# Kernel tuning notes

Hardware: AMD Instinct MI355X
Metric: run time of the kernel (lower is better)

## Reference

```python
import jax, jax.numpy as jnp
import numpy as np

N = 50000
E = 800000
IN = 256
HID = 64
H12 = 4
LAT = 32
NEG_SLOPE = 0.2


def gat_conv(x, src, dst, W, a_src, a_dst, b, heads, out_ch, concat):
    """PyG GATConv (eval mode, add_self_loops already applied to src/dst).
    x: [N, F_in]; src/dst: [Etot]; W: [F_in, heads*out_ch]; a_*: [heads, out_ch]; b: bias.
    Returns (out, alpha[Etot, heads])."""
    n = x.shape[0]
    h = (x @ W).reshape(n, heads, out_ch)                 # [N,H,C]
    e_src = (h * a_src).sum(-1)                           # [N,H]
    e_dst = (h * a_dst).sum(-1)                           # [N,H]
    e = jax.nn.leaky_relu(e_src[src] + e_dst[dst], NEG_SLOPE)   # [Etot,H]
    emax = jax.ops.segment_max(e, dst, num_segments=n)
    ee = jnp.exp(e - emax[dst])
    denom = jax.ops.segment_sum(ee, dst, num_segments=n)
    alpha = ee / (denom[dst] + 1e-16)                     # segment softmax over incoming edges
    msg = h[src] * alpha[:, :, None]                      # [Etot,H,C]
    out = jax.ops.segment_sum(msg, dst, num_segments=n)   # [N,H,C]
    out = out.reshape(n, heads * out_ch) if concat else out.mean(axis=1)
    return out + b, alpha


def setup_inputs() -> dict:
    key = jax.random.key(0)
    ks = jax.random.split(key, 20)
    s = 0.1
    inp = {
        "x": jax.random.normal(ks[0], (N, IN), jnp.float32),
        "edge_index": jax.random.randint(ks[1], (2, E), 0, N, jnp.int32),
        "W1": jax.random.normal(ks[2], (IN, H12 * HID), jnp.float32) * s,
        "a1s": jax.random.normal(ks[3], (H12, HID), jnp.float32) * s,
        "a1d": jax.random.normal(ks[4], (H12, HID), jnp.float32) * s,
        "b1": jnp.zeros((H12 * HID,), jnp.float32),
        "W2": jax.random.normal(ks[5], (H12 * HID, H12 * HID), jnp.float32) * s,
        "a2s": jax.random.normal(ks[6], (H12, HID), jnp.float32) * s,
        "a2d": jax.random.normal(ks[7], (H12, HID), jnp.float32) * s,
        "b2": jnp.zeros((HID,), jnp.float32),
        "Wm": jax.random.normal(ks[8], (HID, LAT), jnp.float32) * s,
        "ams": jax.random.normal(ks[9], (1, LAT), jnp.float32) * s,
        "amd": jax.random.normal(ks[10], (1, LAT), jnp.float32) * s,
        "bm": jnp.zeros((LAT,), jnp.float32),
        # log_std head
        "Ws": jax.random.normal(ks[11], (HID, LAT), jnp.float32) * s,
        "ass": jax.random.normal(ks[12], (1, LAT), jnp.float32) * s,
        "asd": jax.random.normal(ks[13], (1, LAT), jnp.float32) * s,
        "bs": jnp.zeros((LAT,), jnp.float32),
    }
    return inp


def reference(x, edge_index, W1, a1s, a1d, b1, W2, a2s, a2d, b2,
              Wm, ams, amd, bm, Ws, ass, asd, bs):
    # GATConv adds self loops by default
    loops = jnp.arange(N, dtype=edge_index.dtype)
    src = jnp.concatenate([edge_index[0], loops])
    dst = jnp.concatenate([edge_index[1], loops])

    h1, a_w1 = gat_conv(x, src, dst, W1, a1s, a1d, b1, H12, HID, True)
    h1 = jax.nn.relu(h1)
    h2, a_w2 = gat_conv(h1, src, dst, W2, a2s, a2d, b2, H12, HID, False)
    h2 = jax.nn.relu(h2)  # dropout is identity in eval mode
    z_mean, a_wm = gat_conv(h2, src, dst, Wm, ams, amd, bm, 1, LAT, False)
    z_log_std, a_ws = gat_conv(h2, src, dst, Ws, ass, asd, bs, 1, LAT, False)
    return (z_mean, z_log_std, a_w1, a_w2, a_wm, a_ws)
```

## Files before the change

### kernel.cpp

```cpp
#include <hip/hip_runtime.h>
#include <cstdint>
#include <cstddef>

#define NN 50000
#define EE 800000
#define ETOT 850000
#define NEG_SLOPE 0.2f

typedef _Float16 f16;
typedef __attribute__((ext_vector_type(4))) _Float16 f16x4;
typedef __attribute__((ext_vector_type(8))) _Float16 f16x8;
typedef __attribute__((ext_vector_type(4))) float f32x4;


__global__ __launch_bounds__(256) void deg_kernel(const int* __restrict__ ei, int* __restrict__ deg) {
    int e = blockIdx.x * 256 + threadIdx.x;
    if (e >= ETOT) return;
    int d = (e < EE) ? ei[EE + e] : (e - EE);
    atomicAdd(&deg[d], 1);
}

__global__ __launch_bounds__(256) void scan1_kernel(const int* __restrict__ deg, int* __restrict__ offs,
                                                    int* __restrict__ bsum, int n) {
    __shared__ int sh[256];
    int i = blockIdx.x * 256 + threadIdx.x;
    int v = (i < n) ? deg[i] : 0;
    sh[threadIdx.x] = v;
    __syncthreads();
    for (int off = 1; off < 256; off <<= 1) {
        int t = (threadIdx.x >= off) ? sh[threadIdx.x - off] : 0;
        __syncthreads();
        sh[threadIdx.x] += t;
        __syncthreads();
    }
    if (i < n) offs[i] = sh[threadIdx.x] - v;
    if (threadIdx.x == 255) bsum[blockIdx.x] = sh[255];
}

__global__ __launch_bounds__(256) void scan2_kernel(int* __restrict__ bsum, int nb) {
    __shared__ int sh[256];
    int v = (threadIdx.x < nb) ? bsum[threadIdx.x] : 0;
    sh[threadIdx.x] = v;
    __syncthreads();
    for (int off = 1; off < 256; off <<= 1) {
        int t = (threadIdx.x >= off) ? sh[threadIdx.x - off] : 0;
        __syncthreads();
        sh[threadIdx.x] += t;
        __syncthreads();
    }
    if (threadIdx.x < nb) bsum[threadIdx.x] = sh[threadIdx.x] - v;
}

__global__ __launch_bounds__(256) void scan3_kernel(const int* __restrict__ bsum, int* __restrict__ offs,
                                                    int* __restrict__ cursor, int n) {
    int i = blockIdx.x * 256 + threadIdx.x;
    if (i < n) {
        int o = offs[i] + bsum[blockIdx.x];
        offs[i] = o;
        cursor[i] = o;
    }
}

__global__ __launch_bounds__(256) void fill_kernel(const int* __restrict__ ei, int* __restrict__ cursor,
                                                   int* __restrict__ csrc) {
    int e = blockIdx.x * 256 + threadIdx.x;
    if (e >= ETOT) return;
    int d, s;
    if (e < EE) { s = ei[e]; d = ei[EE + e]; } else { s = e - EE; d = e - EE; }
    int p = atomicAdd(&cursor[d], 1);
    csrc[p] = s;
}


template<int K, int NH, bool AF32>
__global__ __launch_bounds__(256) void mfma_gemm_fused(
    const void* __restrict__ Ap, const f16* __restrict__ Bt, f16* __restrict__ C,
    const float* __restrict__ aS, const float* __restrict__ aD,
    float* __restrict__ es, float* __restrict__ ed, int M, int N) {
    int w = threadIdx.x >> 6, lane = threadIdx.x & 63;
    int m0 = blockIdx.y * 128 + w * 32;
    int n0 = blockIdx.x * 64;
    int r = lane & 15, kb = lane >> 4;
    int ar0 = m0 + r;       if (ar0 > M - 1) ar0 = M - 1;
    int ar1 = m0 + 16 + r;  if (ar1 > M - 1) ar1 = M - 1;
    f32x4 acc[2][4] = {};
    const float* Af = (const float*)Ap;
    const f16*   Ah = (const f16*)Ap;
    size_t a0off = (size_t)ar0 * K + kb * 8;
    size_t a1off = (size_t)ar1 * K + kb * 8;
    const f16* bbase = Bt + (size_t)(n0 + r) * K + kb * 8;
    for (int k0 = 0; k0 < K; k0 += 32) {
        f16x8 a0, a1;
        if constexpr (AF32) {
            float4 l0 = *(const float4*)(Af + a0off + k0);
            float4 h0 = *(const float4*)(Af + a0off + k0 + 4);
            float4 l1 = *(const float4*)(Af + a1off + k0);
            float4 h1 = *(const float4*)(Af + a1off + k0 + 4);
            a0[0]=(f16)l0.x; a0[1]=(f16)l0.y; a0[2]=(f16)l0.z; a0[3]=(f16)l0.w;
            a0[4]=(f16)h0.x; a0[5]=(f16)h0.y; a0[6]=(f16)h0.z; a0[7]=(f16)h0.w;
            a1[0]=(f16)l1.x; a1[1]=(f16)l1.y; a1[2]=(f16)l1.z; a1[3]=(f16)l1.w;
            a1[4]=(f16)h1.x; a1[5]=(f16)h1.y; a1[6]=(f16)h1.z; a1[7]=(f16)h1.w;
        } else {
            a0 = *(const f16x8*)(Ah + a0off + k0);
            a1 = *(const f16x8*)(Ah + a1off + k0);
        }
#pragma unroll
        for (int ni = 0; ni < 4; ++ni) {
            f16x8 b = *(const f16x8*)(bbase + (size_t)ni * 16 * K + k0);
            acc[0][ni] = __builtin_amdgcn_mfma_f32_16x16x32_f16(a0, b, acc[0][ni], 0, 0, 0);
            acc[1][ni] = __builtin_amdgcn_mfma_f32_16x16x32_f16(a1, b, acc[1][ni], 0, 0, 0);
        }
    }
    float aSl[4], aDl[4];
#pragma unroll
    for (int ni = 0; ni < 4; ++ni) {
        aSl[ni] = aS[n0 + ni * 16 + r];
        aDl[ni] = aD[n0 + ni * 16 + r];
    }
#pragma unroll
    for (int mi = 0; mi < 2; ++mi) {
#pragma unroll
        for (int i = 0; i < 4; ++i) {
            int row = m0 + mi * 16 + kb * 4 + i;
            bool ok = row < M;
            if (ok) {
#pragma unroll
                for (int ni = 0; ni < 4; ++ni)
                    C[(size_t)row * N + n0 + ni * 16 + r] = (f16)acc[mi][ni][i];
            }
            if constexpr (NH == 4) {
                float pes = acc[mi][0][i] * aSl[0] + acc[mi][1][i] * aSl[1] + acc[mi][2][i] * aSl[2] + acc[mi][3][i] * aSl[3];
                float ped = acc[mi][0][i] * aDl[0] + acc[mi][1][i] * aDl[1] + acc[mi][2][i] * aDl[2] + acc[mi][3][i] * aDl[3];
#pragma unroll
                for (int off = 1; off < 16; off <<= 1) {
                    pes += __shfl_xor(pes, off);
                    ped += __shfl_xor(ped, off);
                }
                if (r == 0 && ok) {
                    es[(size_t)row * 4 + blockIdx.x] = pes;
                    ed[(size_t)row * 4 + blockIdx.x] = ped;
                }
            } else {
                float p0s = acc[mi][0][i] * aSl[0] + acc[mi][1][i] * aSl[1];
                float p1s = acc[mi][2][i] * aSl[2] + acc[mi][3][i] * aSl[3];
                float p0d = acc[mi][0][i] * aDl[0] + acc[mi][1][i] * aDl[1];
                float p1d = acc[mi][2][i] * aDl[2] + acc[mi][3][i] * aDl[3];
#pragma unroll
                for (int off = 1; off < 16; off <<= 1) {
                    p0s += __shfl_xor(p0s, off);
                    p1s += __shfl_xor(p1s, off);
                    p0d += __shfl_xor(p0d, off);
                    p1d += __shfl_xor(p1d, off);
                }
                if (r == 0 && ok) {
                    es[(size_t)row * 2 + 0] = p0s;
                    es[(size_t)row * 2 + 1] = p1s;
                    ed[(size_t)row * 2 + 0] = p0d;
                    ed[(size_t)row * 2 + 1] = p1d;
                }
            }
        }
    }
}


__global__ __launch_bounds__(256) void packw_kernel(const float* __restrict__ W1, const float* __restrict__ W2,
                                                    const float* __restrict__ Wm, const float* __restrict__ Ws,
                                                    const float* __restrict__ ams, const float* __restrict__ ass,
                                                    const float* __restrict__ amd, const float* __restrict__ asd,
                                                    f16* __restrict__ Wt1, f16* __restrict__ Wt2,
                                                    f16* __restrict__ Wtms,
                                                    float* __restrict__ aS, float* __restrict__ aD) {
    int i = blockIdx.x * 256 + threadIdx.x;
    if (i < 65536) {
        int n = i >> 8, k = i & 255;
        Wt1[(size_t)n * 256 + k] = (f16)W1[(size_t)k * 256 + n];
        Wt2[(size_t)n * 256 + k] = (f16)W2[(size_t)k * 256 + n];
    }
    if (i < 4096) {
        int c = i >> 6, k = i & 63;
        float v = (c < 32) ? Wm[k * 32 + c] : Ws[k * 32 + (c - 32)];
        Wtms[(size_t)c * 64 + k] = (f16)v;
    }
    if (i < 64) {
        aS[i] = (i < 32) ? ams[i] : ass[i - 32];
        aD[i] = (i < 32) ? amd[i] : asd[i - 32];
    }
}

__device__ __forceinline__ float leaky(float v) { return v > 0.f ? v : NEG_SLOPE * v; }


__global__ __launch_bounds__(256) void alpha_all_kernel(
    const int* __restrict__ ei,
    const float* __restrict__ es1, const float* __restrict__ ed1, const float* __restrict__ inv1,
    const float* __restrict__ es2, const float* __restrict__ ed2, const float* __restrict__ inv2,
    const float* __restrict__ esms, const float* __restrict__ edms, const float* __restrict__ invms,
    float* __restrict__ aw1, float* __restrict__ aw2,
    float* __restrict__ awm, float* __restrict__ aws) {
    int e = blockIdx.x * 256 + threadIdx.x;
    if (e >= ETOT) return;
    int s, d;
    if (e < EE) { s = ei[e]; d = ei[EE + e]; } else { s = e - EE; d = e - EE; }
    {
        float4 esv = *(const float4*)(es1 + (size_t)s * 4);
        float4 edv = *(const float4*)(ed1 + (size_t)d * 4);
        float4 iv  = *(const float4*)(inv1 + (size_t)d * 4);
        float4 r;
        r.x = __expf(leaky(esv.x + edv.x)) * iv.x;
        r.y = __expf(leaky(esv.y + edv.y)) * iv.y;
        r.z = __expf(leaky(esv.z + edv.z)) * iv.z;
        r.w = __expf(leaky(esv.w + edv.w)) * iv.w;
        *(float4*)(aw1 + (size_t)e * 4) = r;
    }
    {
        float4 esv = *(const float4*)(es2 + (size_t)s * 4);
        float4 edv = *(const float4*)(ed2 + (size_t)d * 4);
        float4 iv  = *(const float4*)(inv2 + (size_t)d * 4);
        float4 r;
        r.x = __expf(leaky(esv.x + edv.x)) * iv.x;
        r.y = __expf(leaky(esv.y + edv.y)) * iv.y;
        r.z = __expf(leaky(esv.z + edv.z)) * iv.z;
        r.w = __expf(leaky(esv.w + edv.w)) * iv.w;
        *(float4*)(aw2 + (size_t)e * 4) = r;
    }
    {
        float2 esv = *(const float2*)(esms + (size_t)s * 2);
        float2 edv = *(const float2*)(edms + (size_t)d * 2);
        float2 iv  = *(const float2*)(invms + (size_t)d * 2);
        awm[e] = __expf(leaky(esv.x + edv.x)) * iv.x;
        aws[e] = __expf(leaky(esv.y + edv.y)) * iv.y;
    }
}


__global__ __launch_bounds__(128) void agg_concat_kernel(
    const f16* __restrict__ H, const float* __restrict__ es, const float* __restrict__ ed,
    const int* __restrict__ offs, const int* __restrict__ csrc,
    const float* __restrict__ bias, f16* __restrict__ out, float* __restrict__ invout) {
    int wave = threadIdx.x >> 6, lane = threadIdx.x & 63;
    int n = blockIdx.x * 2 + wave;
    if (n >= NN) return;
    int start = offs[n];
    int end = (n + 1 < NN) ? offs[n + 1] : ETOT;
    int deg = end - start;
    int h16 = lane >> 4, sub = lane & 15;
    float edh = ed[n * 4 + h16];
    float dsum = 0.f;
    for (int j = sub; j < deg; j += 16) {
        int s = csrc[start + j];
        dsum += __expf(leaky(es[s * 4 + h16] + edh));
    }
    for (int off = 1; off < 16; off <<= 1) dsum += __shfl_xor(dsum, off);
    float inv = 1.f / (dsum + 1e-16f);
    if (sub == 0) invout[n * 4 + h16] = inv;
    int half = lane >> 5;
    int l5 = lane & 31;
    int hh = l5 >> 3;
    int c8 = l5 * 8;
    float invh = __shfl(inv, hh << 4);
    float edhh = __shfl(edh, hh << 4);
    float accv[8] = {};
    int j = half;
    for (; j + 6 < deg; j += 8) {
        int p0 = start + j, p1 = start + j + 2, p2 = start + j + 4, p3 = start + j + 6;
        int s0 = csrc[p0], s1 = csrc[p1], s2 = csrc[p2], s3 = csrc[p3];
        float a0 = __expf(leaky(es[s0 * 4 + hh] + edhh)) * invh;
        float a1 = __expf(leaky(es[s1 * 4 + hh] + edhh)) * invh;
        float a2 = __expf(leaky(es[s2 * 4 + hh] + edhh)) * invh;
        float a3 = __expf(leaky(es[s3 * 4 + hh] + edhh)) * invh;
        f16x8 v0 = *(const f16x8*)(H + (size_t)s0 * 256 + c8);
        f16x8 v1 = *(const f16x8*)(H + (size_t)s1 * 256 + c8);
        f16x8 v2 = *(const f16x8*)(H + (size_t)s2 * 256 + c8);
        f16x8 v3 = *(const f16x8*)(H + (size_t)s3 * 256 + c8);
#pragma unroll
        for (int k = 0; k < 8; ++k)
            accv[k] += a0 * (float)v0[k] + a1 * (float)v1[k] + a2 * (float)v2[k] + a3 * (float)v3[k];
    }
    for (; j < deg; j += 2) {
        int s0 = csrc[start + j];
        float a0 = __expf(leaky(es[s0 * 4 + hh] + edhh)) * invh;
        f16x8 v0 = *(const f16x8*)(H + (size_t)s0 * 256 + c8);
#pragma unroll
        for (int k = 0; k < 8; ++k) accv[k] += a0 * (float)v0[k];
    }
#pragma unroll
    for (int k = 0; k < 8; ++k) accv[k] += __shfl_xor(accv[k], 32);
    if (lane < 32) {
        f16x8 r;
#pragma unroll
        for (int k = 0; k < 8; ++k) r[k] = (f16)fmaxf(accv[k] + bias[c8 + k], 0.f);
        *(f16x8*)(out + (size_t)n * 256 + c8) = r;
    }
}


__global__ __launch_bounds__(128) void agg_mean_kernel(
    const f16* __restrict__ H, const float* __restrict__ es, const float* __restrict__ ed,
    const int* __restrict__ offs, const int* __restrict__ csrc,
    const float* __restrict__ bias, f16* __restrict__ out, float* __restrict__ invout) {
    int wave = threadIdx.x >> 6, lane = threadIdx.x & 63;
    int n = blockIdx.x * 2 + wave;
    if (n >= NN) return;
    int start = offs[n];
    int end = (n + 1 < NN) ? offs[n + 1] : ETOT;
    int deg = end - start;
    int h16 = lane >> 4, sub = lane & 15;
    float edh = ed[n * 4 + h16];
    float dsum = 0.f;
    for (int j = sub; j < deg; j += 16) {
        int s = csrc[start + j];
        dsum += __expf(leaky(es[s * 4 + h16] + edh));
    }
    for (int off = 1; off < 16; off <<= 1) dsum += __shfl_xor(dsum, off);
    float inv = 1.f / (dsum + 1e-16f);
    if (sub == 0) invout[n * 4 + h16] = inv;
    int half = lane >> 5;
    int l5 = lane & 31;
    int hh = l5 >> 3;
    int c8 = l5 * 8;
    float invh = __shfl(inv, hh << 4);
    float edhh = __shfl(edh, hh << 4);
    float accv[8] = {};
    int j = half;
    for (; j + 6 < deg; j += 8) {
        int p0 = start + j, p1 = start + j + 2, p2 = start + j + 4, p3 = start + j + 6;
        int s0 = csrc[p0], s1 = csrc[p1], s2 = csrc[p2], s3 = csrc[p3];
        float a0 = __expf(leaky(es[s0 * 4 + hh] + edhh)) * invh;
        float a1 = __expf(leaky(es[s1 * 4 + hh] + edhh)) * invh;
        float a2 = __expf(leaky(es[s2 * 4 + hh] + edhh)) * invh;
        float a3 = __expf(leaky(es[s3 * 4 + hh] + edhh)) * invh;
        f16x8 v0 = *(const f16x8*)(H + (size_t)s0 * 256 + c8);
        f16x8 v1 = *(const f16x8*)(H + (size_t)s1 * 256 + c8);
        f16x8 v2 = *(const f16x8*)(H + (size_t)s2 * 256 + c8);
        f16x8 v3 = *(const f16x8*)(H + (size_t)s3 * 256 + c8);
#pragma unroll
        for (int k = 0; k < 8; ++k)
            accv[k] += a0 * (float)v0[k] + a1 * (float)v1[k] + a2 * (float)v2[k] + a3 * (float)v3[k];
    }
    for (; j < deg; j += 2) {
        int s0 = csrc[start + j];
        float a0 = __expf(leaky(es[s0 * 4 + hh] + edhh)) * invh;
        f16x8 v0 = *(const f16x8*)(H + (size_t)s0 * 256 + c8);
#pragma unroll
        for (int k = 0; k < 8; ++k) accv[k] += a0 * (float)v0[k];
    }
#pragma unroll
    for (int k = 0; k < 8; ++k) {
        accv[k] += __shfl_xor(accv[k], 8);
        accv[k] += __shfl_xor(accv[k], 16);
        accv[k] += __shfl_xor(accv[k], 32);
    }
    if (lane < 8) {
        f16x8 r;
#pragma unroll
        for (int k = 0; k < 8; ++k) r[k] = (f16)fmaxf(accv[k] * 0.25f + bias[lane * 8 + k], 0.f);
        *(f16x8*)(out + (size_t)n * 64 + lane * 8) = r;
    }
}


__global__ __launch_bounds__(128) void agg_ms_kernel(
    const f16* __restrict__ H, const float* __restrict__ es, const float* __restrict__ ed,
    const int* __restrict__ offs, const int* __restrict__ csrc,
    const float* __restrict__ bm, const float* __restrict__ bs,
    float* __restrict__ zmean, float* __restrict__ zlog, float* __restrict__ invout) {
    int wave = threadIdx.x >> 6, lane = threadIdx.x & 63;
    int n = blockIdx.x * 2 + wave;
    if (n >= NN) return;
    int start = offs[n];
    int end = (n + 1 < NN) ? offs[n + 1] : ETOT;
    int deg = end - start;
    int g = lane >> 5, sub = lane & 31;
    float edg = ed[n * 2 + g];
    float dsum = 0.f;
    for (int j = sub; j < deg; j += 32) {
        int s = csrc[start + j];
        dsum += __expf(leaky(es[s * 2 + g] + edg));
    }
    for (int off = 1; off < 32; off <<= 1) dsum += __shfl_xor(dsum, off);
    float inv = 1.f / (dsum + 1e-16f);
    if (sub == 0) invout[n * 2 + g] = inv;
    int slot = lane >> 3;
    int le = lane & 7;
    int g2 = le >> 2;
    int c8 = le * 8;
    float invg = __shfl(inv, g2 << 5);
    float edg2 = __shfl(edg, g2 << 5);
    float accv[8] = {};
    for (int j = slot; j < deg; j += 8) {
        int p = start + j;
        int s = csrc[p];
        float a = __expf(leaky(es[s * 2 + g2] + edg2)) * invg;
        f16x8 v = *(const f16x8*)(H + (size_t)s * 64 + c8);
#pragma unroll
        for (int k = 0; k < 8; ++k) accv[k] += a * (float)v[k];
    }
#pragma unroll
    for (int k = 0; k < 8; ++k) {
        accv[k] += __shfl_xor(accv[k], 8);
        accv[k] += __shfl_xor(accv[k], 16);
        accv[k] += __shfl_xor(accv[k], 32);
    }
    if (lane < 4) {
        float4 r0, r1;
        int cb = lane * 8;
        r0.x = accv[0] + bm[cb + 0]; r0.y = accv[1] + bm[cb + 1];
        r0.z = accv[2] + bm[cb + 2]; r0.w = accv[3] + bm[cb + 3];
        r1.x = accv[4] + bm[cb + 4]; r1.y = accv[5] + bm[cb + 5];
        r1.z = accv[6] + bm[cb + 6]; r1.w = accv[7] + bm[cb + 7];
        *(float4*)(zmean + (size_t)n * 32 + cb) = r0;
        *(float4*)(zmean + (size_t)n * 32 + cb + 4) = r1;
    } else if (lane < 8) {
        float4 r0, r1;
        int cb = (lane - 4) * 8;
        r0.x = accv[0] + bs[cb + 0]; r0.y = accv[1] + bs[cb + 1];
        r0.z = accv[2] + bs[cb + 2]; r0.w = accv[3] + bs[cb + 3];
        r1.x = accv[4] + bs[cb + 4]; r1.y = accv[5] + bs[cb + 5];
        r1.z = accv[6] + bs[cb + 6]; r1.w = accv[7] + bs[cb + 7];
        *(float4*)(zlog + (size_t)n * 32 + cb) = r0;
        *(float4*)(zlog + (size_t)n * 32 + cb + 4) = r1;
    }
}


extern "C" void kernel_launch(void* const* d_in, const int* in_sizes, int n_in,
                              void* d_out, int out_size, void* d_ws, size_t ws_size,
                              hipStream_t stream) {
    const float* x   = (const float*)d_in[0];
    const int*   ei  = (const int*)d_in[1];
    const float* W1  = (const float*)d_in[2];
    const float* a1s = (const float*)d_in[3];
    const float* a1d = (const float*)d_in[4];
    const float* b1  = (const float*)d_in[5];
    const float* W2  = (const float*)d_in[6];
    const float* a2s = (const float*)d_in[7];
    const float* a2d = (const float*)d_in[8];
    const float* b2  = (const float*)d_in[9];
    const float* Wm  = (const float*)d_in[10];
    const float* ams = (const float*)d_in[11];
    const float* amd = (const float*)d_in[12];
    const float* bm  = (const float*)d_in[13];
    const float* Ws  = (const float*)d_in[14];
    const float* ass = (const float*)d_in[15];
    const float* asd = (const float*)d_in[16];
    const float* bs  = (const float*)d_in[17];

    float* out = (float*)d_out;
    float* zmean = out;
    float* zlog  = out + 1600000;
    float* a_w1  = out + 3200000;
    float* a_w2  = out + 6600000;
    float* a_wm  = out + 10000000;
    float* a_ws_o = out + 10850000;

    float* ws = (float*)d_ws;
    size_t o = 0;
    f16*   Hh   = (f16*)(ws + o); o += (size_t)NN * 128;
    f16*   h1h  = (f16*)(ws + o); o += (size_t)NN * 128;
    f16*   h2h  = (f16*)(ws + o); o += (size_t)NN * 32;
    float* es1  = ws + o; o += NN * 4;
    float* ed1  = ws + o; o += NN * 4;
    float* es2  = ws + o; o += NN * 4;
    float* ed2  = ws + o; o += NN * 4;
    float* esms = ws + o; o += NN * 2;
    float* edms = ws + o; o += NN * 2;
    float* inv1 = ws + o; o += NN * 4;
    float* inv2 = ws + o; o += NN * 4;
    float* invms= ws + o; o += NN * 2;
    f16*   Wt1  = (f16*)(ws + o); o += 32768;
    f16*   Wt2  = (f16*)(ws + o); o += 32768;
    f16*   Wtms = (f16*)(ws + o); o += 2048;
    float* aSms = ws + o; o += 64;
    float* aDms = ws + o; o += 64;
    int* deg    = (int*)(ws + o); o += NN;
    int* offs   = (int*)(ws + o); o += NN;
    int* cursor = (int*)(ws + o); o += NN;
    int* csrc   = (int*)(ws + o); o += ETOT;

    const int edgeBlocks = (ETOT + 255) / 256;
    const int nodeBlocks = (NN + 255) / 256;
    const int aggBlocks  = (NN + 1) / 2;

    hipMemsetAsync(deg, 0, NN * sizeof(int), stream);
    deg_kernel<<<edgeBlocks, 256, 0, stream>>>(ei, deg);
    scan1_kernel<<<nodeBlocks, 256, 0, stream>>>(deg, offs, cursor , NN);
    scan2_kernel<<<1, 256, 0, stream>>>(cursor, nodeBlocks);
    scan3_kernel<<<nodeBlocks, 256, 0, stream>>>(cursor, offs, deg , NN);
    fill_kernel<<<edgeBlocks, 256, 0, stream>>>(ei, deg, csrc);

    packw_kernel<<<256, 256, 0, stream>>>(W1, W2, Wm, Ws, ams, ass, amd, asd, Wt1, Wt2, Wtms, aSms, aDms);

    dim3 gg1(4, (NN + 127) / 128);
    dim3 gg3(1, (NN + 127) / 128);
    mfma_gemm_fused<256, 4, true><<<gg1, 256, 0, stream>>>(x, Wt1, Hh, a1s, a1d, es1, ed1, NN, 256);
    agg_concat_kernel<<<aggBlocks, 128, 0, stream>>>(Hh, es1, ed1, offs, csrc, b1, h1h, inv1);

    mfma_gemm_fused<256, 4, false><<<gg1, 256, 0, stream>>>(h1h, Wt2, Hh, a2s, a2d, es2, ed2, NN, 256);
    agg_mean_kernel<<<aggBlocks, 128, 0, stream>>>(Hh, es2, ed2, offs, csrc, b2, h2h, inv2);

    mfma_gemm_fused<64, 2, false><<<gg3, 256, 0, stream>>>(h2h, Wtms, Hh, aSms, aDms, esms, edms, NN, 64);
    agg_ms_kernel<<<aggBlocks, 128, 0, stream>>>(Hh, esms, edms, offs, csrc, bm, bs,
                                                 zmean, zlog, invms);

    alpha_all_kernel<<<edgeBlocks, 256, 0, stream>>>(ei, es1, ed1, inv1, es2, ed2, inv2,
                                                     esms, edms, invms, a_w1, a_w2, a_wm, a_ws_o);
}
```

Baseline: 545.1 us.

## Fuse per-layer alpha output into next GEMM grid and interleave ed/inv storage

The monolithic alpha kernel that ran after all layers is split up. Layer-1 and layer-2 attention weights are now computed by extra blocks appended to the next layer's GEMM grid, so that edge work overlaps with the MFMA GEMM. The ed and inv arrays are interleaved per node, so one cache line serves both gathers. Aggregation kernels drop to one wave per block. The cost is a larger GEMM launch with branch-divergent block roles, and smaller blocks that raise block-scheduling overhead.

```diff
diff --git a/kernel.cpp b/kernel.cpp
--- a/kernel.cpp
+++ b/kernel.cpp
@@ -8,7 +8,6 @@
 #define NEG_SLOPE 0.2f
 
 typedef _Float16 f16;
-typedef __attribute__((ext_vector_type(4))) _Float16 f16x4;
 typedef __attribute__((ext_vector_type(8))) _Float16 f16x8;
 typedef __attribute__((ext_vector_type(4))) float f32x4;
 
@@ -71,12 +70,34 @@
     csrc[p] = s;
 }
 
-
-template<int K, int NH, bool AF32>
+__device__ __forceinline__ float leaky(float v) { return v > 0.f ? v : NEG_SLOPE * v; }
+
+
+template<int K, int NH, bool AF32, int ALPHA_NH>
 __global__ __launch_bounds__(256) void mfma_gemm_fused(
     const void* __restrict__ Ap, const f16* __restrict__ Bt, f16* __restrict__ C,
     const float* __restrict__ aS, const float* __restrict__ aD,
-    float* __restrict__ es, float* __restrict__ ed, int M, int N) {
+    float* __restrict__ es, float* __restrict__ edi, int M, int N, int RB,
+    const int* __restrict__ ei, const float* __restrict__ esA,
+    const float* __restrict__ ediA, float* __restrict__ awA) {
+    if ((int)blockIdx.y >= RB) {
+        if constexpr (ALPHA_NH == 4) {
+            int e = (((int)blockIdx.y - RB) * (int)gridDim.x + (int)blockIdx.x) * 256 + (int)threadIdx.x;
+            if (e >= ETOT) return;
+            int s, d;
+            if (e < EE) { s = ei[e]; d = ei[EE + e]; } else { s = e - EE; d = e - EE; }
+            float4 esv = *(const float4*)(esA + (size_t)s * 4);
+            float4 edv = *(const float4*)(ediA + (size_t)d * 8);
+            float4 iv  = *(const float4*)(ediA + (size_t)d * 8 + 4);
+            float4 r;
+            r.x = __expf(leaky(esv.x + edv.x)) * iv.x;
+            r.y = __expf(leaky(esv.y + edv.y)) * iv.y;
+            r.z = __expf(leaky(esv.z + edv.z)) * iv.z;
+            r.w = __expf(leaky(esv.w + edv.w)) * iv.w;
+            *(float4*)(awA + (size_t)e * 4) = r;
+        }
+        return;
+    }
     int w = threadIdx.x >> 6, lane = threadIdx.x & 63;
     int m0 = blockIdx.y * 128 + w * 32;
     int n0 = blockIdx.x * 64;
@@ -138,7 +159,7 @@
                 }
                 if (r == 0 && ok) {
                     es[(size_t)row * 4 + blockIdx.x] = pes;
-                    ed[(size_t)row * 4 + blockIdx.x] = ped;
+                    edi[(size_t)row * 8 + blockIdx.x] = ped;
                 }
             } else {
                 float p0s = acc[mi][0][i] * aSl[0] + acc[mi][1][i] * aSl[1];
@@ -155,8 +176,8 @@
                 if (r == 0 && ok) {
                     es[(size_t)row * 2 + 0] = p0s;
                     es[(size_t)row * 2 + 1] = p1s;
-                    ed[(size_t)row * 2 + 0] = p0d;
-                    ed[(size_t)row * 2 + 1] = p1d;
+                    edi[(size_t)row * 4 + 0] = p0d;
+                    edi[(size_t)row * 4 + 1] = p1d;
                 }
             }
         }
@@ -188,64 +209,33 @@
     }
 }
 
-__device__ __forceinline__ float leaky(float v) { return v > 0.f ? v : NEG_SLOPE * v; }
-
-
-__global__ __launch_bounds__(256) void alpha_all_kernel(
-    const int* __restrict__ ei,
-    const float* __restrict__ es1, const float* __restrict__ ed1, const float* __restrict__ inv1,
-    const float* __restrict__ es2, const float* __restrict__ ed2, const float* __restrict__ inv2,
-    const float* __restrict__ esms, const float* __restrict__ edms, const float* __restrict__ invms,
-    float* __restrict__ aw1, float* __restrict__ aw2,
-    float* __restrict__ awm, float* __restrict__ aws) {
+
+__global__ __launch_bounds__(256) void alpha_ms_kernel(const int* __restrict__ ei, const float* __restrict__ es,
+                                                       const float* __restrict__ edi,
+                                                       float* __restrict__ awm, float* __restrict__ aws) {
     int e = blockIdx.x * 256 + threadIdx.x;
     if (e >= ETOT) return;
     int s, d;
     if (e < EE) { s = ei[e]; d = ei[EE + e]; } else { s = e - EE; d = e - EE; }
-    {
-        float4 esv = *(const float4*)(es1 + (size_t)s * 4);
-        float4 edv = *(const float4*)(ed1 + (size_t)d * 4);
-        float4 iv  = *(const float4*)(inv1 + (size_t)d * 4);
-        float4 r;
-        r.x = __expf(leaky(esv.x + edv.x)) * iv.x;
-        r.y = __expf(leaky(esv.y + edv.y)) * iv.y;
-        r.z = __expf(leaky(esv.z + edv.z)) * iv.z;
-        r.w = __expf(leaky(esv.w + edv.w)) * iv.w;
-        *(float4*)(aw1 + (size_t)e * 4) = r;
-    }
-    {
-        float4 esv = *(const float4*)(es2 + (size_t)s * 4);
-        float4 edv = *(const float4*)(ed2 + (size_t)d * 4);
-        float4 iv  = *(const float4*)(inv2 + (size_t)d * 4);
-        float4 r;
-        r.x = __expf(leaky(esv.x + edv.x)) * iv.x;
-        r.y = __expf(leaky(esv.y + edv.y)) * iv.y;
-        r.z = __expf(leaky(esv.z + edv.z)) * iv.z;
-        r.w = __expf(leaky(esv.w + edv.w)) * iv.w;
-        *(float4*)(aw2 + (size_t)e * 4) = r;
-    }
-    {
-        float2 esv = *(const float2*)(esms + (size_t)s * 2);
-        float2 edv = *(const float2*)(edms + (size_t)d * 2);
-        float2 iv  = *(const float2*)(invms + (size_t)d * 2);
-        awm[e] = __expf(leaky(esv.x + edv.x)) * iv.x;
-        aws[e] = __expf(leaky(esv.y + edv.y)) * iv.y;
-    }
-}
-
-
-__global__ __launch_bounds__(128) void agg_concat_kernel(
-    const f16* __restrict__ H, const float* __restrict__ es, const float* __restrict__ ed,
+    float2 esv = *(const float2*)(es + (size_t)s * 2);
+    float2 edv = *(const float2*)(edi + (size_t)d * 4);
+    float2 iv  = *(const float2*)(edi + (size_t)d * 4 + 2);
+    awm[e] = __expf(leaky(esv.x + edv.x)) * iv.x;
+    aws[e] = __expf(leaky(esv.y + edv.y)) * iv.y;
+}
+
+
+__global__ __launch_bounds__(64) void agg_concat_kernel(
+    const f16* __restrict__ H, const float* __restrict__ es, float* __restrict__ edi,
     const int* __restrict__ offs, const int* __restrict__ csrc,
-    const float* __restrict__ bias, f16* __restrict__ out, float* __restrict__ invout) {
-    int wave = threadIdx.x >> 6, lane = threadIdx.x & 63;
-    int n = blockIdx.x * 2 + wave;
-    if (n >= NN) return;
+    const float* __restrict__ bias, f16* __restrict__ out) {
+    int lane = threadIdx.x;
+    int n = blockIdx.x;
     int start = offs[n];
     int end = (n + 1 < NN) ? offs[n + 1] : ETOT;
     int deg = end - start;
     int h16 = lane >> 4, sub = lane & 15;
-    float edh = ed[n * 4 + h16];
+    float edh = edi[(size_t)n * 8 + h16];
     float dsum = 0.f;
     for (int j = sub; j < deg; j += 16) {
         int s = csrc[start + j];
@@ -253,7 +243,7 @@
     }
     for (int off = 1; off < 16; off <<= 1) dsum += __shfl_xor(dsum, off);
     float inv = 1.f / (dsum + 1e-16f);
-    if (sub == 0) invout[n * 4 + h16] = inv;
+    if (sub == 0) edi[(size_t)n * 8 + 4 + h16] = inv;
     int half = lane >> 5;
     int l5 = lane & 31;
     int hh = l5 >> 3;
@@ -295,18 +285,17 @@
 }
 
 
-__global__ __launch_bounds__(128) void agg_mean_kernel(
-    const f16* __restrict__ H, const float* __restrict__ es, const float* __restrict__ ed,
+__global__ __launch_bounds__(64) void agg_mean_kernel(
+    const f16* __restrict__ H, const float* __restrict__ es, float* __restrict__ edi,
     const int* __restrict__ offs, const int* __restrict__ csrc,
-    const float* __restrict__ bias, f16* __restrict__ out, float* __restrict__ invout) {
-    int wave = threadIdx.x >> 6, lane = threadIdx.x & 63;
-    int n = blockIdx.x * 2 + wave;
-    if (n >= NN) return;
+    const float* __restrict__ bias, f16* __restrict__ out) {
+    int lane = threadIdx.x;
+    int n = blockIdx.x;
     int start = offs[n];
     int end = (n + 1 < NN) ? offs[n + 1] : ETOT;
     int deg = end - start;
     int h16 = lane >> 4, sub = lane & 15;
-    float edh = ed[n * 4 + h16];
+    float edh = edi[(size_t)n * 8 + h16];
     float dsum = 0.f;
     for (int j = sub; j < deg; j += 16) {
         int s = csrc[start + j];
@@ -314,7 +303,7 @@
     }
     for (int off = 1; off < 16; off <<= 1) dsum += __shfl_xor(dsum, off);
     float inv = 1.f / (dsum + 1e-16f);
-    if (sub == 0) invout[n * 4 + h16] = inv;
+    if (sub == 0) edi[(size_t)n * 8 + 4 + h16] = inv;
     int half = lane >> 5;
     int l5 = lane & 31;
     int hh = l5 >> 3;
@@ -360,19 +349,18 @@
 }
 
 
-__global__ __launch_bounds__(128) void agg_ms_kernel(
-    const f16* __restrict__ H, const float* __restrict__ es, const float* __restrict__ ed,
+__global__ __launch_bounds__(64) void agg_ms_kernel(
+    const f16* __restrict__ H, const float* __restrict__ es, float* __restrict__ edi,
     const int* __restrict__ offs, const int* __restrict__ csrc,
     const float* __restrict__ bm, const float* __restrict__ bs,
-    float* __restrict__ zmean, float* __restrict__ zlog, float* __restrict__ invout) {
-    int wave = threadIdx.x >> 6, lane = threadIdx.x & 63;
-    int n = blockIdx.x * 2 + wave;
-    if (n >= NN) return;
+    float* __restrict__ zmean, float* __restrict__ zlog) {
+    int lane = threadIdx.x;
+    int n = blockIdx.x;
     int start = offs[n];
     int end = (n + 1 < NN) ? offs[n + 1] : ETOT;
     int deg = end - start;
     int g = lane >> 5, sub = lane & 31;
-    float edg = ed[n * 2 + g];
+    float edg = edi[(size_t)n * 4 + g];
     float dsum = 0.f;
     for (int j = sub; j < deg; j += 32) {
         int s = csrc[start + j];
@@ -380,7 +368,7 @@
     }
     for (int off = 1; off < 32; off <<= 1) dsum += __shfl_xor(dsum, off);
     float inv = 1.f / (dsum + 1e-16f);
-    if (sub == 0) invout[n * 2 + g] = inv;
+    if (sub == 0) edi[(size_t)n * 4 + 2 + g] = inv;
     int slot = lane >> 3;
     int le = lane & 7;
     int g2 = le >> 2;
@@ -460,14 +448,11 @@
     f16*   h1h  = (f16*)(ws + o); o += (size_t)NN * 128;
     f16*   h2h  = (f16*)(ws + o); o += (size_t)NN * 32;
     float* es1  = ws + o; o += NN * 4;
-    float* ed1  = ws + o; o += NN * 4;
     float* es2  = ws + o; o += NN * 4;
-    float* ed2  = ws + o; o += NN * 4;
     float* esms = ws + o; o += NN * 2;
-    float* edms = ws + o; o += NN * 2;
-    float* inv1 = ws + o; o += NN * 4;
-    float* inv2 = ws + o; o += NN * 4;
-    float* invms= ws + o; o += NN * 2;
+    float* edi1 = ws + o; o += NN * 8;
+    float* edi2 = ws + o; o += NN * 8;
+    float* edims= ws + o; o += NN * 4;
     f16*   Wt1  = (f16*)(ws + o); o += 32768;
     f16*   Wt2  = (f16*)(ws + o); o += 32768;
     f16*   Wtms = (f16*)(ws + o); o += 2048;
@@ -480,7 +465,7 @@
 
     const int edgeBlocks = (ETOT + 255) / 256;
     const int nodeBlocks = (NN + 255) / 256;
-    const int aggBlocks  = (NN + 1) / 2;
+    const int RB = (NN + 127) / 128;
 
     hipMemsetAsync(deg, 0, NN * sizeof(int), stream);
     deg_kernel<<<edgeBlocks, 256, 0, stream>>>(ei, deg);
@@ -491,18 +476,21 @@
 
     packw_kernel<<<256, 256, 0, stream>>>(W1, W2, Wm, Ws, ams, ass, amd, asd, Wt1, Wt2, Wtms, aSms, aDms);
 
-    dim3 gg1(4, (NN + 127) / 128);
-    dim3 gg3(1, (NN + 127) / 128);
-    mfma_gemm_fused<256, 4, true><<<gg1, 256, 0, stream>>>(x, Wt1, Hh, a1s, a1d, es1, ed1, NN, 256);
-    agg_concat_kernel<<<aggBlocks, 128, 0, stream>>>(Hh, es1, ed1, offs, csrc, b1, h1h, inv1);
-
-    mfma_gemm_fused<256, 4, false><<<gg1, 256, 0, stream>>>(h1h, Wt2, Hh, a2s, a2d, es2, ed2, NN, 256);
-    agg_mean_kernel<<<aggBlocks, 128, 0, stream>>>(Hh, es2, ed2, offs, csrc, b2, h2h, inv2);
-
-    mfma_gemm_fused<64, 2, false><<<gg3, 256, 0, stream>>>(h2h, Wtms, Hh, aSms, aDms, esms, edms, NN, 64);
-    agg_ms_kernel<<<aggBlocks, 128, 0, stream>>>(Hh, esms, edms, offs, csrc, bm, bs,
-                                                 zmean, zlog, invms);
-
-    alpha_all_kernel<<<edgeBlocks, 256, 0, stream>>>(ei, es1, ed1, inv1, es2, ed2, inv2,
-                                                     esms, edms, invms, a_w1, a_w2, a_wm, a_ws_o);
-}
+    dim3 gg1(4, RB);
+    dim3 gg2(4, RB + (edgeBlocks + 3) / 4);
+    dim3 gg3(1, RB + edgeBlocks);
+
+    mfma_gemm_fused<256, 4, true, 0><<<gg1, 256, 0, stream>>>(
+        x, Wt1, Hh, a1s, a1d, es1, edi1, NN, 256, RB, nullptr, nullptr, nullptr, nullptr);
+    agg_concat_kernel<<<NN, 64, 0, stream>>>(Hh, es1, edi1, offs, csrc, b1, h1h);
+
+    mfma_gemm_fused<256, 4, false, 4><<<gg2, 256, 0, stream>>>(
+        h1h, Wt2, Hh, a2s, a2d, es2, edi2, NN, 256, RB, ei, es1, edi1, a_w1);
+    agg_mean_kernel<<<NN, 64, 0, stream>>>(Hh, es2, edi2, offs, csrc, b2, h2h);
+
+    mfma_gemm_fused<64, 2, false, 4><<<gg3, 256, 0, stream>>>(
+        h2h, Wtms, Hh, aSms, aDms, esms, edims, NN, 64, RB, ei, es2, edi2, a_w2);
+    agg_ms_kernel<<<NN, 64, 0, stream>>>(Hh, esms, edims, offs, csrc, bm, bs, zmean, zlog);
+
+    alpha_ms_kernel<<<edgeBlocks, 256, 0, stream>>>(ei, esms, edims, a_wm, a_ws_o);
+}
```

Result: faster. 511.8 us (-6.1%).
